# Kernel tuning notes

Hardware: AMD Instinct MI355X
Metric: run time of the kernel (lower is better)

Reference implementation:

```python
import jax, jax.numpy as jnp
import numpy as np

K = 2  # top-k experts per token


def setup_inputs() -> dict:
    key = jax.random.key(0)
    kx, kw = jax.random.split(key)
    N, D, E = 16384, 4096, 64
    x = jax.random.normal(kx, (N, D), dtype=jnp.float32)
    # nn.Linear(input_dim, num_experts, bias=False) weight: [num_experts, input_dim]
    W = jax.random.normal(kw, (E, D), dtype=jnp.float32) * (1.0 / np.sqrt(D))
    return {"x": x, "W": W}


def reference(x, W):
    # logits = x @ W^T : [N, E]
    logits = jnp.einsum('nd,ed->ne', x, W)
    top_k_logits, top_k_indices = jax.lax.top_k(logits, K)  # [N, K]
    top_k_weights = jax.nn.softmax(top_k_logits, axis=-1)   # softmax over the k selected
    N = logits.shape[0]
    rows = jnp.arange(N)[:, None]  # [N, 1] broadcast against [N, K]
    full_weights = jnp.zeros_like(logits).at[rows, top_k_indices].set(top_k_weights)
    return full_weights, top_k_indices
```

## Files before the change

kernel.cpp:

```cpp
#include <hip/hip_runtime.h>
#include <math.h>

#define N_TOK 16384
#define DDIM  4096
#define NEXP  64
#define TM    32
#define WINF  256
#define NSTEP (DDIM / WINF)
#define LSTR  68
#define TAU   1e-3f

typedef __attribute__((ext_vector_type(8))) short bf16x8;
typedef __attribute__((ext_vector_type(4))) float f32x4;

__device__ __forceinline__ void split8(f32x4 v0, f32x4 v1, bf16x8& hi, bf16x8& lo) {
    float f[8];
    *(f32x4*)&f[0] = v0;  *(f32x4*)&f[4] = v1;
    #pragma unroll
    for (int i = 0; i < 8; ++i) {
        unsigned u  = __float_as_uint(f[i]);
        unsigned uh = u & 0xFFFF0000u;
        float    rf = f[i] - __uint_as_float(uh);
        hi[i] = (short)(u >> 16);
        lo[i] = (short)(__float_as_uint(rf) >> 16);
    }
}

__device__ __forceinline__ void gl2lds16(const void* g, void* l) {
    __builtin_amdgcn_global_load_lds(
        (const __attribute__((address_space(1))) unsigned int*)g,
        (__attribute__((address_space(3))) unsigned int*)l,
        16, 0, 0);
}

__global__ __launch_bounds__(256) void pack_w_kernel(
    const float* __restrict__ W, short* __restrict__ Wp)
{
    const int c    = blockIdx.x;
    const int tid  = threadIdx.x;
    const int t    = tid >> 6;
    const int lane = tid & 63;
    const int r16  = lane & 15;
    const int koct = lane >> 4;
    const float* src = W + (size_t)(t * 16 + r16) * DDIM + c * 32 + koct * 8;
    f32x4 b0 = *(const f32x4*)src;
    f32x4 b1 = *(const f32x4*)(src + 4);
    bf16x8 hi, lo;
    split8(b0, b1, hi, lo);
    short* d = Wp + ((size_t)(c * 4 + t) * 2) * 512 + lane * 8;
    *(bf16x8*)d         = hi;
    *(bf16x8*)(d + 512) = lo;
}

__global__ __launch_bounds__(512, 2) void topk_gate_kernel(
    const float* __restrict__ x, const short* __restrict__ Wp,
    const float* __restrict__ W, float* __restrict__ out)
{
    __shared__ __align__(16) char sraw[4 * 32768];
    __shared__ int    top_i[TM * 2];
    __shared__ float  top_w[TM * 2];
    __shared__ int    nflag;
    __shared__ int    flist[TM];
    __shared__ double lgd[NEXP];
    __shared__ int    rbi[2];
    __shared__ float  rbw[2];

    const int tid  = threadIdx.x;
    const int lane = tid & 63;
    const int w    = tid >> 6;
    const int block_tok = blockIdx.x * TM;

    if (w >= 4) {
        const int p = w - 4;
        const char* xs[8];
        #pragma unroll
        for (int j = 0; j < 8; ++j)
            xs[j] = (const char*)x
                  + (size_t)(block_tok + p * 8 + j) * (DDIM * 4)
                  + ((lane * 16) ^ (j << 4));
        const int drow = p * 8 * 1024;

#define STAGE(S) do {                                                        \
        char* _d = sraw + (((S) & 3) << 15) + drow;                          \
        const size_t _o = (size_t)(S) * 1024;                                \
        _Pragma("unroll")                                                    \
        for (int j = 0; j < 8; ++j)                                          \
            gl2lds16(xs[j] + _o, _d + j * 1024);                             \
    } while (0)

        STAGE(0); STAGE(1); STAGE(2);
        asm volatile("s_waitcnt vmcnt(16)" ::: "memory");
        __builtin_amdgcn_s_barrier();
        #pragma unroll 1
        for (int s = 0; s < NSTEP - 3; ++s) {
            STAGE(s + 3);
            asm volatile("s_waitcnt vmcnt(16)" ::: "memory");
            __builtin_amdgcn_s_barrier();
        }
        asm volatile("s_waitcnt vmcnt(8)" ::: "memory");
        __builtin_amdgcn_s_barrier();
        asm volatile("s_waitcnt vmcnt(0)" ::: "memory");
        __builtin_amdgcn_s_barrier();
        __builtin_amdgcn_s_barrier();
#undef STAGE
    } else {
        const int h    = w;
        const int r16  = lane & 15;
        const int koct = lane >> 4;
        const int m    = (r16 & 7) << 4;

        f32x4 acc[2][4];
        #pragma unroll
        for (int tt = 0; tt < 2; ++tt)
            #pragma unroll
            for (int t = 0; t < 4; ++t) acc[tt][t] = (f32x4){0.f, 0.f, 0.f, 0.f};

        __syncthreads();
        #pragma unroll 2
        for (int s = 0; s < NSTEP; ++s) {
            const char* buf = sraw + ((s & 3) << 15);
            #pragma unroll
            for (int cc = 0; cc < 2; ++cc) {
                const int c  = h * 2 + cc;
                const int cg = s * 8 + c;
                const int o0 = c * 128 + koct * 32;
                bf16x8 ah[2], al[2];
                #pragma unroll
                for (int tt = 0; tt < 2; ++tt) {
                    const char* xb = buf + ((tt * 16 + r16) << 10);
                    f32x4 a0 = *(const f32x4*)(xb + (o0 ^ m));
                    f32x4 a1 = *(const f32x4*)(xb + ((o0 + 16) ^ m));
                    split8(a0, a1, ah[tt], al[tt]);
                }
                #pragma unroll
                for (int t = 0; t < 4; ++t) {
                    const short* wb = Wp + ((size_t)(cg * 4 + t) * 2) * 512 + lane * 8;
                    bf16x8 bh = *(const bf16x8*)wb;
                    bf16x8 bl = *(const bf16x8*)(wb + 512);
                    #pragma unroll
                    for (int tt = 0; tt < 2; ++tt) {
                        acc[tt][t] = __builtin_amdgcn_mfma_f32_16x16x32_bf16(ah[tt], bh, acc[tt][t], 0, 0, 0);
                        acc[tt][t] = __builtin_amdgcn_mfma_f32_16x16x32_bf16(ah[tt], bl, acc[tt][t], 0, 0, 0);
                        acc[tt][t] = __builtin_amdgcn_mfma_f32_16x16x32_bf16(al[tt], bh, acc[tt][t], 0, 0, 0);
                    }
                }
            }
            __syncthreads();
        }
        float* Lg = (float*)sraw;
        #pragma unroll
        for (int tt = 0; tt < 2; ++tt)
            #pragma unroll
            for (int t = 0; t < 4; ++t)
                #pragma unroll
                for (int r = 0; r < 4; ++r)
                    Lg[(h * TM + tt * 16 + koct * 4 + r) * LSTR + t * 16 + r16] = acc[tt][t][r];
    }

    if (tid == 0) nflag = 0;
    __syncthreads();

    float* Lg = (float*)sraw;
    {
        const int tok = tid >> 4;
        const int e4  = (tid & 15) * 4;
        float4 s0 = *(float4*)&Lg[(0 * TM + tok) * LSTR + e4];
        #pragma unroll
        for (int qq = 1; qq < 4; ++qq) {
            float4 v = *(float4*)&Lg[(qq * TM + tok) * LSTR + e4];
            s0.x += v.x; s0.y += v.y; s0.z += v.z; s0.w += v.w;
        }
        *(float4*)&Lg[tok * LSTR + e4] = s0;
    }
    __syncthreads();

    if (tid < TM) {
        float m1 = -INFINITY, m2 = -INFINITY, m3 = -INFINITY;
        int i1 = 0, i2 = 0;
        for (int e = 0; e < NEXP; ++e) {
            float v = Lg[tid * LSTR + e];
            if (v > m1)      { m3 = m2; m2 = m1; i2 = i1; m1 = v; i1 = e; }
            else if (v > m2) { m3 = m2; m2 = v; i2 = e; }
            else if (v > m3) { m3 = v; }
        }
        float d  = expf(m2 - m1);
        float rn = 1.0f / (1.0f + d);
        top_i[tid * 2 + 0] = i1;  top_i[tid * 2 + 1] = i2;
        top_w[tid * 2 + 0] = rn;  top_w[tid * 2 + 1] = d * rn;
        float2* oi = (float2*)(out + (size_t)N_TOK * NEXP);
        oi[block_tok + tid] = make_float2((float)i1, (float)i2);
        if ((m1 - m2 < TAU) || (m2 - m3 < TAU)) {
            int pp = atomicAdd(&nflag, 1);
            flist[pp] = tid;
        }
    }
    __syncthreads();

    {
        float4* ow = (float4*)(out + (size_t)block_tok * NEXP);
        const int tok = tid >> 4;
        const int e4  = (tid & 15) * 4;
        int a1 = top_i[tok * 2], a2 = top_i[tok * 2 + 1];
        float v1 = top_w[tok * 2], v2 = top_w[tok * 2 + 1];
        float4 v; float* vp = (float*)&v;
        #pragma unroll
        for (int q = 0; q < 4; ++q) {
            int e = e4 + q;
            vp[q] = (e == a1) ? v1 : ((e == a2) ? v2 : 0.0f);
        }
        ow[tid] = v;
    }
    __syncthreads();

    double* red = (double*)(sraw + 40960);
    const int fn = nflag;
    for (int f = 0; f < fn; ++f) {
        const int tok = block_tok + flist[f];
        {
            const int e = tid & 63, q = tid >> 6;
            const float* wr = W + (size_t)e * DDIM + q * (DDIM / 8);
            const float* xr = x + (size_t)tok * DDIM + q * (DDIM / 8);
            double pp = 0.0;
            for (int k = 0; k < DDIM / 8; k += 4) {
                float4 wv = *(const float4*)(wr + k);
                float4 xv = *(const float4*)(xr + k);
                pp += (double)xv.x * (double)wv.x;
                pp += (double)xv.y * (double)wv.y;
                pp += (double)xv.z * (double)wv.z;
                pp += (double)xv.w * (double)wv.w;
            }
            red[tid] = pp;
        }
        __syncthreads();
        if (tid < 64) {
            double s = 0.0;
            #pragma unroll
            for (int j = 0; j < 8; ++j) s += red[tid + 64 * j];
            lgd[tid] = s;
        }
        __syncthreads();

        if (tid == 0) {
            double m1 = -INFINITY, m2 = -INFINITY;
            int i1 = 0, i2 = 0;
            for (int ee = 0; ee < NEXP; ++ee) {
                double v = lgd[ee];
                if (v > m1)      { m2 = m1; i2 = i1; m1 = v; i1 = ee; }
                else if (v > m2) { m2 = v; i2 = ee; }
            }
            double d  = exp(m2 - m1);
            double rn = 1.0 / (1.0 + d);
            rbi[0] = i1; rbi[1] = i2;
            rbw[0] = (float)rn; rbw[1] = (float)(d * rn);
            float2* oi = (float2*)(out + (size_t)N_TOK * NEXP);
            oi[tok] = make_float2((float)i1, (float)i2);
        }
        __syncthreads();

        if (tid < 16) {
            float4 v = make_float4(0.f, 0.f, 0.f, 0.f);
            float* vp = (float*)&v;
            #pragma unroll
            for (int qq = 0; qq < 4; ++qq) {
                int ee = tid * 4 + qq;
                if (ee == rbi[0]) vp[qq] = rbw[0];
                else if (ee == rbi[1]) vp[qq] = rbw[1];
            }
            ((float4*)(out + (size_t)tok * NEXP))[tid] = v;
        }
        __syncthreads();
    }
}

extern "C" void kernel_launch(void* const* d_in, const int* in_sizes, int n_in,
                              void* d_out, int out_size, void* d_ws, size_t ws_size,
                              hipStream_t stream) {
    const float* x = (const float*)d_in[0];
    const float* W = (const float*)d_in[1];
    float* out = (float*)d_out;
    short* Wp  = (short*)d_ws;
    (void)in_sizes; (void)n_in; (void)ws_size; (void)out_size;

    hipLaunchKernelGGL(pack_w_kernel, dim3(DDIM / 32), dim3(256), 0, stream, W, Wp);
    hipLaunchKernelGGL(topk_gate_kernel, dim3(N_TOK / TM), dim3(512), 0, stream,
                       x, Wp, W, out);
}
```

Measured before the change: 494.9 us.

## Replace producer/consumer warp split with register-staged double buffering across all warps

Removes the dedicated loader warps that used global_load_lds with a 4-stage LDS ring, and instead has all 8 warps load x into registers, write them to a 2-buffer LDS ring, and run MFMA compute on one k-chunk each. LDS use drops from 128KB to 72KB and launch bounds raise occupancy to 4 blocks, with the partial-logit reduction extended from 4 to 8 partials. This trades asynchronous direct-to-LDS copies and deeper prefetch for more compute warps and occupancy, but adds extra syncthreads per step and register pressure under the tighter launch bound.

```diff
diff --git a/kernel.cpp b/kernel.cpp
--- a/kernel.cpp
+++ b/kernel.cpp
@@ -24,13 +24,6 @@
         hi[i] = (short)(u >> 16);
         lo[i] = (short)(__float_as_uint(rf) >> 16);
     }
-}
-
-__device__ __forceinline__ void gl2lds16(const void* g, void* l) {
-    __builtin_amdgcn_global_load_lds(
-        (const __attribute__((address_space(1))) unsigned int*)g,
-        (__attribute__((address_space(3))) unsigned int*)l,
-        16, 0, 0);
 }
 
 __global__ __launch_bounds__(256) void pack_w_kernel(
@@ -52,11 +45,11 @@
     *(bf16x8*)(d + 512) = lo;
 }
 
-__global__ __launch_bounds__(512, 2) void topk_gate_kernel(
+__global__ __launch_bounds__(512, 4) void topk_gate_kernel(
     const float* __restrict__ x, const short* __restrict__ Wp,
     const float* __restrict__ W, float* __restrict__ out)
 {
-    __shared__ __align__(16) char sraw[4 * 32768];
+    __shared__ __align__(16) char sraw[73728];
     __shared__ int    top_i[TM * 2];
     __shared__ float  top_w[TM * 2];
     __shared__ int    nflag;
@@ -69,104 +62,104 @@
     const int lane = tid & 63;
     const int w    = tid >> 6;
     const int block_tok = blockIdx.x * TM;
-
-    if (w >= 4) {
-        const int p = w - 4;
-        const char* xs[8];
-        #pragma unroll
-        for (int j = 0; j < 8; ++j)
-            xs[j] = (const char*)x
-                  + (size_t)(block_tok + p * 8 + j) * (DDIM * 4)
-                  + ((lane * 16) ^ (j << 4));
-        const int drow = p * 8 * 1024;
-
-#define STAGE(S) do {                                                        \
-        char* _d = sraw + (((S) & 3) << 15) + drow;                          \
-        const size_t _o = (size_t)(S) * 1024;                                \
+    const int r16  = lane & 15;
+    const int koct = lane >> 4;
+    const int m    = (r16 & 7) << 4;
+    const int o0   = w * 128 + koct * 32;
+
+    const char* xrow = (const char*)x
+                     + (size_t)(block_tok + w * 4) * (DDIM * 4) + lane * 16;
+    const int sw0 = (lane * 16) ^ ((((w * 4) + 0) & 7) << 4);
+    const int sw1 = (lane * 16) ^ ((((w * 4) + 1) & 7) << 4);
+    const int sw2 = (lane * 16) ^ ((((w * 4) + 2) & 7) << 4);
+    const int sw3 = (lane * 16) ^ ((((w * 4) + 3) & 7) << 4);
+    char* const wbase = sraw + (w * 4) * 1024;
+
+    f32x4 rA0, rA1, rA2, rA3, rB0, rB1, rB2, rB3;
+
+#define LOADR(a0, a1, a2, a3, S) do {                                        \
+    const char* _s = xrow + (size_t)(S) * 1024;                              \
+    a0 = *(const f32x4*)(_s);                                                \
+    a1 = *(const f32x4*)(_s + 16384);                                        \
+    a2 = *(const f32x4*)(_s + 32768);                                        \
+    a3 = *(const f32x4*)(_s + 49152);                                        \
+} while (0)
+
+#define WRITER(a0, a1, a2, a3, B) do {                                       \
+    char* _d = wbase + (B) * 32768;                                          \
+    *(f32x4*)(_d +        sw0) = a0;                                         \
+    *(f32x4*)(_d + 1024 + sw1) = a1;                                         \
+    *(f32x4*)(_d + 2048 + sw2) = a2;                                         \
+    *(f32x4*)(_d + 3072 + sw3) = a3;                                         \
+} while (0)
+
+    f32x4 acc[2][4];
+    #pragma unroll
+    for (int tt = 0; tt < 2; ++tt)
+        #pragma unroll
+        for (int t = 0; t < 4; ++t) acc[tt][t] = (f32x4){0.f, 0.f, 0.f, 0.f};
+
+#define COMPUTE(B, S) do {                                                   \
+    const char* _buf = sraw + (B) * 32768;                                   \
+    const int _cg = (S) * 8 + w;                         \
+    bf16x8 ah[2], al[2];                                                     \
+    _Pragma("unroll")                                                        \
+    for (int tt = 0; tt < 2; ++tt) {                                         \
+        const char* xb = _buf + ((tt * 16 + r16) << 10);                     \
+        f32x4 a0 = *(const f32x4*)(xb + (o0 ^ m));                           \
+        f32x4 a1 = *(const f32x4*)(xb + ((o0 + 16) ^ m));                    \
+        split8(a0, a1, ah[tt], al[tt]);                                      \
+    }                                                                        \
+    _Pragma("unroll")                                                        \
+    for (int t = 0; t < 4; ++t) {                                            \
+        const short* wb = Wp + ((size_t)(_cg * 4 + t) * 2) * 512 + lane * 8; \
+        bf16x8 bh = *(const bf16x8*)wb;                                      \
+        bf16x8 bl = *(const bf16x8*)(wb + 512);                              \
         _Pragma("unroll")                                                    \
-        for (int j = 0; j < 8; ++j)                                          \
-            gl2lds16(xs[j] + _o, _d + j * 1024);                             \
-    } while (0)
-
-        STAGE(0); STAGE(1); STAGE(2);
-        asm volatile("s_waitcnt vmcnt(16)" ::: "memory");
-        __builtin_amdgcn_s_barrier();
-        #pragma unroll 1
-        for (int s = 0; s < NSTEP - 3; ++s) {
-            STAGE(s + 3);
-            asm volatile("s_waitcnt vmcnt(16)" ::: "memory");
-            __builtin_amdgcn_s_barrier();
-        }
-        asm volatile("s_waitcnt vmcnt(8)" ::: "memory");
-        __builtin_amdgcn_s_barrier();
-        asm volatile("s_waitcnt vmcnt(0)" ::: "memory");
-        __builtin_amdgcn_s_barrier();
-        __builtin_amdgcn_s_barrier();
-#undef STAGE
-    } else {
-        const int h    = w;
-        const int r16  = lane & 15;
-        const int koct = lane >> 4;
-        const int m    = (r16 & 7) << 4;
-
-        f32x4 acc[2][4];
-        #pragma unroll
-        for (int tt = 0; tt < 2; ++tt)
+        for (int tt = 0; tt < 2; ++tt) {                                     \
+            acc[tt][t] = __builtin_amdgcn_mfma_f32_16x16x32_bf16(ah[tt], bh, acc[tt][t], 0, 0, 0); \
+            acc[tt][t] = __builtin_amdgcn_mfma_f32_16x16x32_bf16(ah[tt], bl, acc[tt][t], 0, 0, 0); \
+            acc[tt][t] = __builtin_amdgcn_mfma_f32_16x16x32_bf16(al[tt], bh, acc[tt][t], 0, 0, 0); \
+        }                                                                    \
+    }                                                                        \
+} while (0)
+
+    LOADR(rA0, rA1, rA2, rA3, 0);
+    LOADR(rB0, rB1, rB2, rB3, 1);
+    #pragma unroll 1
+    for (int s = 0; s < NSTEP; s += 2) {
+        WRITER(rA0, rA1, rA2, rA3, 0);
+        __syncthreads();
+        if (s + 2 < NSTEP) LOADR(rA0, rA1, rA2, rA3, s + 2);
+        COMPUTE(0, s);
+        __syncthreads();
+        WRITER(rB0, rB1, rB2, rB3, 1);
+        __syncthreads();
+        if (s + 3 < NSTEP) LOADR(rB0, rB1, rB2, rB3, s + 3);
+        COMPUTE(1, s + 1);
+        __syncthreads();
+    }
+#undef LOADR
+#undef WRITER
+#undef COMPUTE
+
+    float* Lg = (float*)sraw;
+    #pragma unroll
+    for (int tt = 0; tt < 2; ++tt)
+        #pragma unroll
+        for (int t = 0; t < 4; ++t)
             #pragma unroll
-            for (int t = 0; t < 4; ++t) acc[tt][t] = (f32x4){0.f, 0.f, 0.f, 0.f};
-
-        __syncthreads();
-        #pragma unroll 2
-        for (int s = 0; s < NSTEP; ++s) {
-            const char* buf = sraw + ((s & 3) << 15);
-            #pragma unroll
-            for (int cc = 0; cc < 2; ++cc) {
-                const int c  = h * 2 + cc;
-                const int cg = s * 8 + c;
-                const int o0 = c * 128 + koct * 32;
-                bf16x8 ah[2], al[2];
-                #pragma unroll
-                for (int tt = 0; tt < 2; ++tt) {
-                    const char* xb = buf + ((tt * 16 + r16) << 10);
-                    f32x4 a0 = *(const f32x4*)(xb + (o0 ^ m));
-                    f32x4 a1 = *(const f32x4*)(xb + ((o0 + 16) ^ m));
-                    split8(a0, a1, ah[tt], al[tt]);
-                }
-                #pragma unroll
-                for (int t = 0; t < 4; ++t) {
-                    const short* wb = Wp + ((size_t)(cg * 4 + t) * 2) * 512 + lane * 8;
-                    bf16x8 bh = *(const bf16x8*)wb;
-                    bf16x8 bl = *(const bf16x8*)(wb + 512);
-                    #pragma unroll
-                    for (int tt = 0; tt < 2; ++tt) {
-                        acc[tt][t] = __builtin_amdgcn_mfma_f32_16x16x32_bf16(ah[tt], bh, acc[tt][t], 0, 0, 0);
-                        acc[tt][t] = __builtin_amdgcn_mfma_f32_16x16x32_bf16(ah[tt], bl, acc[tt][t], 0, 0, 0);
-                        acc[tt][t] = __builtin_amdgcn_mfma_f32_16x16x32_bf16(al[tt], bh, acc[tt][t], 0, 0, 0);
-                    }
-                }
-            }
-            __syncthreads();
-        }
-        float* Lg = (float*)sraw;
-        #pragma unroll
-        for (int tt = 0; tt < 2; ++tt)
-            #pragma unroll
-            for (int t = 0; t < 4; ++t)
-                #pragma unroll
-                for (int r = 0; r < 4; ++r)
-                    Lg[(h * TM + tt * 16 + koct * 4 + r) * LSTR + t * 16 + r16] = acc[tt][t][r];
-    }
-
+            for (int r = 0; r < 4; ++r)
+                Lg[(w * TM + tt * 16 + koct * 4 + r) * LSTR + t * 16 + r16] = acc[tt][t][r];
     if (tid == 0) nflag = 0;
     __syncthreads();
 
-    float* Lg = (float*)sraw;
     {
         const int tok = tid >> 4;
         const int e4  = (tid & 15) * 4;
         float4 s0 = *(float4*)&Lg[(0 * TM + tok) * LSTR + e4];
         #pragma unroll
-        for (int qq = 1; qq < 4; ++qq) {
+        for (int qq = 1; qq < 8; ++qq) {
             float4 v = *(float4*)&Lg[(qq * TM + tok) * LSTR + e4];
             s0.x += v.x; s0.y += v.y; s0.z += v.z; s0.w += v.w;
         }
@@ -212,7 +205,7 @@
     }
     __syncthreads();
 
-    double* red = (double*)(sraw + 40960);
+    double* red = (double*)(sraw + 69632);
     const int fn = nflag;
     for (int f = 0; f < fn; ++f) {
         const int tok = block_tok + flist[f];
```

New measurement: 511.2 us. 1.03x slower.
